# Kernel tuning notes

Hardware: AMD Instinct MI355X
Metric: run time of the kernel (lower is better)

Reference implementation:

```python
import jax, jax.numpy as jnp
import numpy as np

WIN = 7  # window side

def _relative_position_index(wh, ww):
    coords = np.stack(np.meshgrid(np.arange(wh), np.arange(ww), indexing='ij'))  # (2,wh,ww)
    coords = coords.reshape(2, -1)                       # (2, S)
    rel = coords[:, :, None] - coords[:, None, :]        # (2, S, S)
    rel = rel.transpose(1, 2, 0).copy()                  # (S, S, 2)
    rel[:, :, 0] += wh - 1
    rel[:, :, 1] += ww - 1
    rel[:, :, 0] *= 2 * ww - 1
    return rel.sum(-1).astype(np.int32)                  # (S, S)

def setup_inputs() -> dict:
    key = jax.random.key(0)
    ks = jax.random.split(key, 8)
    B_, S, D, H = 4096, WIN * WIN, 384, 6
    Wn = 64  # windows per image
    x = jax.random.normal(ks[0], (B_, S, D), dtype=jnp.float32)
    mask = jax.random.normal(ks[1], (Wn, S, S), dtype=jnp.float32)
    qkv_w = jax.random.normal(ks[2], (D, 3 * D), dtype=jnp.float32) * (D ** -0.5)
    qkv_b = jnp.zeros((3 * D,), dtype=jnp.float32)
    proj_w = jax.random.normal(ks[3], (D, D), dtype=jnp.float32) * (D ** -0.5)
    proj_b = jnp.zeros((D,), dtype=jnp.float32)
    bias_table = jax.random.normal(ks[4], ((2 * WIN - 1) ** 2, H), dtype=jnp.float32) * 0.02
    rel_index = jnp.asarray(_relative_position_index(WIN, WIN))  # (S, S) int32
    return {"x": x, "mask": mask, "qkv_w": qkv_w, "qkv_b": qkv_b,
            "proj_w": proj_w, "proj_b": proj_b, "bias_table": bias_table,
            "rel_index": rel_index}

def reference(x, mask, qkv_w, qkv_b, proj_w, proj_b, bias_table, rel_index):
    B_, S, D = x.shape
    H = bias_table.shape[1]
    hd = D // H
    scale = hd ** -0.5
    qkv = x @ qkv_w + qkv_b                              # (B_, S, 3D)
    qkv = qkv.reshape(B_, S, 3, H, hd).transpose(2, 0, 3, 1, 4)  # (3, B_, H, S, hd)
    q, k, v = qkv[0], qkv[1], qkv[2]
    attn = jnp.einsum('bhqe,bhke->bhqk', q * scale, k)   # (B_, H, S, S)
    bias = bias_table[rel_index].transpose(2, 0, 1)      # (H, S, S)
    attn = attn + bias[None]
    Wn = mask.shape[0]
    attn = attn.reshape(B_ // Wn, Wn, H, S, S) + mask[None, :, None]
    attn = jax.nn.softmax(attn.reshape(B_, H, S, S), axis=-1)
    out = jnp.einsum('bhqk,bhke->bhqe', attn, v)         # (B_, H, S, hd)
    out = out.transpose(0, 2, 1, 3).reshape(B_, S, D)
    return out @ proj_w + proj_b
```

## Files before the change

kernel.cpp:

```cpp
#include <hip/hip_runtime.h>


typedef __attribute__((ext_vector_type(8))) short bfx8;
typedef __attribute__((ext_vector_type(4))) float fx4;

typedef const __attribute__((address_space(1))) void* gptr_t;
typedef __attribute__((address_space(3))) void* lptr_t;

__device__ __forceinline__ short f2bf(float f) {
  union { float f; unsigned u; } v;
  v.f = f;
  unsigned r = v.u + 0x7fffu + ((v.u >> 16) & 1u);
  return (short)(r >> 16);
}


__global__ __launch_bounds__(256) void convT_kernel(const float* __restrict__ w,
                                                    short* __restrict__ wt, int N, int K) {
  int i = blockIdx.x * 256 + threadIdx.x;
  if (i < N * K) {
    int n = i / K, k = i - n * K;
    wt[i] = f2bf(w[(size_t)k * N + n]);
  }
}

__global__ __launch_bounds__(256) void bm_kernel(const float* __restrict__ mask,
                                                 const float* __restrict__ bias_table,
                                                 const int* __restrict__ rel_index,
                                                 float* __restrict__ bm) {
  int i = blockIdx.x * 256 + threadIdx.x;
  if (i < 64 * 6 * 2401) {
    int rc = i % 2401;
    int wh = i / 2401;
    int h = wh % 6, w = wh / 6;
    bm[i] = bias_table[rel_index[rc] * 6 + h] + mask[w * 2401 + rc];
  }
}


__global__ __launch_bounds__(256, 3) void fused_attn_kernel(
    const float* __restrict__ x,
    const short* __restrict__ wqkv_t,
    const float* __restrict__ qkv_b,
    const float* __restrict__ bm,
    short* __restrict__ O) {
  __shared__ __align__(16) short Qs[64 * 72];
  __shared__ __align__(16) short Ks[64 * 72];
  __shared__ __align__(16) short Vt[64 * 72];
  __shared__ __align__(16) short Pb[6144];
  __shared__ __align__(16) short Ws[6144];

  const int tid = threadIdx.x;
  const int lane = tid & 63, wid = tid >> 6;
  const int l15 = lane & 15, q4 = lane >> 4;
  const int b = blockIdx.x, w = b & 63;
  const float* xw = x + (size_t)b * 49 * 384;
  const float* bmp_base = bm + ((size_t)(w * 6)) * 2401;

  const fx4 zero = {0.f, 0.f, 0.f, 0.f};
  const int arow = wid * 16 + l15;
  const int crow = wid * 16 + q4 * 4;

  auto stage = [&](short* dst, int h64s, int kts) {
#pragma unroll
    for (int r = 0; r < 3; ++r) {
      const int off = r * 4096 + tid * 16;
      const int srow = off >> 6;
      const int ce = (off & 63) >> 1;
      const int n = (srow >> 6) * 384 + h64s + (srow & 63);
      __builtin_amdgcn_global_load_lds(
          (gptr_t)(wqkv_t + (size_t)n * 384 + kts * 32 + ce),
          (lptr_t)((char*)dst + off), 16, 0, 0);
    }
  };

  bfx8 af_all[12];
#pragma unroll
  for (int kt = 0; kt < 12; ++kt) {
    float4 a0 = {0.f, 0.f, 0.f, 0.f}, a1 = {0.f, 0.f, 0.f, 0.f};
    if (arow < 49) {
      const float4* ap = (const float4*)(xw + (size_t)arow * 384 + kt * 32 + q4 * 8);
      a0 = ap[0];
      a1 = ap[1];
    }
    bfx8 af;
    af[0] = f2bf(a0.x); af[1] = f2bf(a0.y); af[2] = f2bf(a0.z); af[3] = f2bf(a0.w);
    af[4] = f2bf(a1.x); af[5] = f2bf(a1.y); af[6] = f2bf(a1.z); af[7] = f2bf(a1.w);
    af_all[kt] = af;
  }

  stage(Ws, 0, 0);

  for (int h = 0; h < 6; ++h) {
    const int h64 = h * 64;
    __syncthreads();

    fx4 qacc[12];
#pragma unroll
    for (int i = 0; i < 12; ++i) qacc[i] = zero;

#pragma unroll
    for (int kt = 0; kt < 12; ++kt) {
      short* sb = (kt & 1) ? Ws : Pb;
      const short* rb = (kt & 1) ? Pb : Ws;
      if (kt < 11) stage(sb, h64, kt + 1);
      const bfx8 af = af_all[kt];
#pragma unroll
      for (int nt = 0; nt < 12; ++nt) {
        const bfx8 bf = *(const bfx8*)&rb[(nt * 16 + l15) * 32 + q4 * 8];
        qacc[nt] = __builtin_amdgcn_mfma_f32_16x16x32_bf16(af, bf, qacc[nt], 0, 0, 0);
      }
      __syncthreads();
    }

#pragma unroll
    for (int nt = 0; nt < 12; ++nt) {
      const int which = nt >> 2;
      const int e = (nt & 3) * 16 + l15;
      const float bias = qkv_b[which * 384 + h64 + e];
      const float sc = (which == 0) ? 0.125f : 1.0f;
#pragma unroll
      for (int rr = 0; rr < 4; ++rr) {
        const int row = crow + rr;
        const short v = f2bf((qacc[nt][rr] + bias) * sc);
        if (which == 0)      Qs[row * 72 + e] = v;
        else if (which == 1) Ks[row * 72 + e] = v;
        else                 Vt[e * 72 + row] = v;
      }
    }
    __syncthreads();

    if (h < 5) stage(Ws, h64 + 64, 0);

    const float* bmp = bmp_base + (size_t)h * 2401;
    float bmv[4][4];
#pragma unroll
    for (int nt = 0; nt < 4; ++nt) {
      const int c = nt * 16 + l15;
#pragma unroll
      for (int rr = 0; rr < 4; ++rr) {
        const int r = crow + rr;
        bmv[nt][rr] = (r < 49 && c < 49) ? bmp[r * 49 + c] : -1e30f;
      }
    }

    fx4 sacc[4];
#pragma unroll
    for (int i = 0; i < 4; ++i) sacc[i] = zero;
#pragma unroll
    for (int ks = 0; ks < 2; ++ks) {
      const bfx8 aq = *(const bfx8*)&Qs[arow * 72 + ks * 32 + q4 * 8];
#pragma unroll
      for (int nt = 0; nt < 4; ++nt) {
        const bfx8 bk = *(const bfx8*)&Ks[(nt * 16 + l15) * 72 + ks * 32 + q4 * 8];
        sacc[nt] = __builtin_amdgcn_mfma_f32_16x16x32_bf16(aq, bk, sacc[nt], 0, 0, 0);
      }
    }

    float p[4][4], mx[4], sm[4];
#pragma unroll
    for (int rr = 0; rr < 4; ++rr) mx[rr] = -1e30f;
#pragma unroll
    for (int nt = 0; nt < 4; ++nt)
#pragma unroll
      for (int rr = 0; rr < 4; ++rr) {
        p[nt][rr] = sacc[nt][rr] + bmv[nt][rr];
        mx[rr] = fmaxf(mx[rr], p[nt][rr]);
      }
#pragma unroll
    for (int rr = 0; rr < 4; ++rr) {
      mx[rr] = fmaxf(mx[rr], __shfl_xor(mx[rr], 1));
      mx[rr] = fmaxf(mx[rr], __shfl_xor(mx[rr], 2));
      mx[rr] = fmaxf(mx[rr], __shfl_xor(mx[rr], 4));
      mx[rr] = fmaxf(mx[rr], __shfl_xor(mx[rr], 8));
      sm[rr] = 0.f;
    }
#pragma unroll
    for (int nt = 0; nt < 4; ++nt)
#pragma unroll
      for (int rr = 0; rr < 4; ++rr) {
        const float e = __expf(p[nt][rr] - mx[rr]);
        p[nt][rr] = e;
        sm[rr] += e;
      }
#pragma unroll
    for (int rr = 0; rr < 4; ++rr) {
      sm[rr] += __shfl_xor(sm[rr], 1);
      sm[rr] += __shfl_xor(sm[rr], 2);
      sm[rr] += __shfl_xor(sm[rr], 4);
      sm[rr] += __shfl_xor(sm[rr], 8);
      sm[rr] = 1.f / sm[rr];
    }
#pragma unroll
    for (int nt = 0; nt < 4; ++nt)
#pragma unroll
      for (int rr = 0; rr < 4; ++rr)
        Pb[(crow + rr) * 72 + nt * 16 + l15] = f2bf(p[nt][rr] * sm[rr]);

    fx4 oacc[4];
#pragma unroll
    for (int i = 0; i < 4; ++i) oacc[i] = zero;
#pragma unroll
    for (int ks = 0; ks < 2; ++ks) {
      const bfx8 ap = *(const bfx8*)&Pb[arow * 72 + ks * 32 + q4 * 8];
#pragma unroll
      for (int nt = 0; nt < 4; ++nt) {
        const bfx8 bv = *(const bfx8*)&Vt[(nt * 16 + l15) * 72 + ks * 32 + q4 * 8];
        oacc[nt] = __builtin_amdgcn_mfma_f32_16x16x32_bf16(ap, bv, oacc[nt], 0, 0, 0);
      }
    }
#pragma unroll
    for (int nt = 0; nt < 4; ++nt)
#pragma unroll
      for (int rr = 0; rr < 4; ++rr) {
        const int r = crow + rr;
        if (r < 49)
          O[((size_t)b * 49 + r) * 384 + h64 + nt * 16 + l15] = f2bf(oacc[nt][rr]);
      }
  }
}


__global__ __launch_bounds__(256) void proj_kernel(
    const short* __restrict__ O,
    const short* __restrict__ wproj_t,
    const float* __restrict__ proj_b,
    float* __restrict__ out) {
  __shared__ __align__(16) short As[128 * 32];
  __shared__ __align__(16) short Bs[128 * 32];

  const int tid = threadIdx.x;
  const int lane = tid & 63, wid = tid >> 6;
  const int l15 = lane & 15, q4 = lane >> 4;
  const int tn = blockIdx.x % 3, tm = blockIdx.x / 3;
  const int wr = wid >> 1, wc = wid & 1;

  const short* Abase = O + (size_t)tm * 128 * 384;
  const short* Bbase = wproj_t + (size_t)tn * 128 * 384;

  fx4 acc[4][4];
#pragma unroll
  for (int i = 0; i < 4; ++i)
#pragma unroll
    for (int j = 0; j < 4; ++j) acc[i][j] = (fx4){0.f, 0.f, 0.f, 0.f};

  for (int kt = 0; kt < 12; ++kt) {
#pragma unroll
    for (int g = 0; g < 2; ++g) {
      const int off = g * 4096 + tid * 16;
      const int row = off >> 6;
      const int ce = (off & 63) >> 1;
      __builtin_amdgcn_global_load_lds(
          (gptr_t)(Abase + (size_t)row * 384 + kt * 32 + ce),
          (lptr_t)((char*)As + off), 16, 0, 0);
      __builtin_amdgcn_global_load_lds(
          (gptr_t)(Bbase + (size_t)row * 384 + kt * 32 + ce),
          (lptr_t)((char*)Bs + off), 16, 0, 0);
    }
    __syncthreads();
    bfx8 a[4], bf[4];
#pragma unroll
    for (int mi = 0; mi < 4; ++mi)
      a[mi] = *(const bfx8*)&As[(wr * 64 + mi * 16 + l15) * 32 + q4 * 8];
#pragma unroll
    for (int ni = 0; ni < 4; ++ni)
      bf[ni] = *(const bfx8*)&Bs[(wc * 64 + ni * 16 + l15) * 32 + q4 * 8];
#pragma unroll
    for (int mi = 0; mi < 4; ++mi)
#pragma unroll
      for (int ni = 0; ni < 4; ++ni)
        acc[mi][ni] = __builtin_amdgcn_mfma_f32_16x16x32_bf16(a[mi], bf[ni], acc[mi][ni], 0, 0, 0);
    __syncthreads();
  }

#pragma unroll
  for (int ni = 0; ni < 4; ++ni) {
    const int gn = tn * 128 + wc * 64 + ni * 16 + l15;
    const float bias = proj_b[gn];
#pragma unroll
    for (int mi = 0; mi < 4; ++mi) {
      const size_t gm = (size_t)tm * 128 + wr * 64 + mi * 16 + q4 * 4;
#pragma unroll
      for (int rr = 0; rr < 4; ++rr)
        out[(gm + rr) * 384 + gn] = acc[mi][ni][rr] + bias;
    }
  }
}


extern "C" void kernel_launch(void* const* d_in, const int* in_sizes, int n_in,
                              void* d_out, int out_size, void* d_ws, size_t ws_size,
                              hipStream_t stream) {
  const float* x       = (const float*)d_in[0];
  const float* mask    = (const float*)d_in[1];
  const float* qkv_w   = (const float*)d_in[2];
  const float* qkv_b   = (const float*)d_in[3];
  const float* proj_w  = (const float*)d_in[4];
  const float* proj_b  = (const float*)d_in[5];
  const float* bias_t  = (const float*)d_in[6];
  const int*   rel_idx = (const int*)d_in[7];
  float* out = (float*)d_out;

  char* ws = (char*)d_ws;
  short* wqkv_t  = (short*)(ws);
  short* wproj_t = (short*)(ws + 884736);
  float* bmw     = (float*)(ws + 884736 + 294912);
  short* O_ws    = (short*)(ws + 884736 + 294912 + 3687936);

  convT_kernel<<<1728, 256, 0, stream>>>(qkv_w, wqkv_t, 1152, 384);
  convT_kernel<<<576, 256, 0, stream>>>(proj_w, wproj_t, 384, 384);
  bm_kernel<<<3602, 256, 0, stream>>>(mask, bias_t, rel_idx, bmw);

  fused_attn_kernel<<<4096, 256, 0, stream>>>(x, wqkv_t, qkv_b, bmw, O_ws);
  proj_kernel<<<4704, 256, 0, stream>>>(O_ws, wproj_t, proj_b, out);
}
```

Baseline: 1.125 ms.

## Restructure fused attention QKV GEMM to keep weights in registers and x in LDS

The QKV projection is restructured: each wave now owns 16 output columns per Q/K/V and holds the full K-dimension weight fragments in registers, loading the next head's weights directly from global memory instead of staging through LDS. The input window x is converted to bf16 once into a swizzled LDS buffer that every wave reads. LDS tiles switch from padded 72-stride to XOR-swizzled 64-stride layouts to avoid bank conflicts, and barriers become explicit lgkmcnt waits plus s_barrier. The per-K-step barriers are removed, but register pressure rises sharply (36 bfx8 weight fragments), occupancy is lowered from 3 to 2 blocks, and the row-48 handling uses an extra broadcast load.

Result: slower. 2.061 ms (+83.2%).

```diff
diff --git a/kernel.cpp b/kernel.cpp
--- a/kernel.cpp
+++ b/kernel.cpp
@@ -2,6 +2,7 @@
 
 
 typedef __attribute__((ext_vector_type(8))) short bfx8;
+typedef __attribute__((ext_vector_type(4))) short bfx4;
 typedef __attribute__((ext_vector_type(4))) float fx4;
 
 typedef const __attribute__((address_space(1))) void* gptr_t;
@@ -13,6 +14,13 @@
   unsigned r = v.u + 0x7fffu + ((v.u >> 16) & 1u);
   return (short)(r >> 16);
 }
+
+#define LGKM_BARRIER()                                 \
+  do {                                                 \
+    asm volatile("s_waitcnt lgkmcnt(0)" ::: "memory"); \
+    __builtin_amdgcn_s_barrier();                      \
+    asm volatile("" ::: "memory");                     \
+  } while (0)
 
 
 __global__ __launch_bounds__(256) void convT_kernel(const float* __restrict__ w,
@@ -38,122 +46,128 @@
 }
 
 
-__global__ __launch_bounds__(256, 3) void fused_attn_kernel(
+__global__ __launch_bounds__(256, 2) void fused_attn_kernel(
     const float* __restrict__ x,
     const short* __restrict__ wqkv_t,
     const float* __restrict__ qkv_b,
     const float* __restrict__ bm,
     short* __restrict__ O) {
-  __shared__ __align__(16) short Qs[64 * 72];
-  __shared__ __align__(16) short Ks[64 * 72];
-  __shared__ __align__(16) short Vt[64 * 72];
-  __shared__ __align__(16) short Pb[6144];
-  __shared__ __align__(16) short Ws[6144];
+  __shared__ __align__(16) short xbf[49 * 384];
+  __shared__ __align__(16) short Qs[64 * 64];
+  __shared__ __align__(16) short Ks[64 * 64];
+  __shared__ __align__(16) short Vt[64 * 64];
+  __shared__ __align__(16) short Pb[64 * 64];
 
   const int tid = threadIdx.x;
   const int lane = tid & 63, wid = tid >> 6;
   const int l15 = lane & 15, q4 = lane >> 4;
   const int b = blockIdx.x, w = b & 63;
   const float* xw = x + (size_t)b * 49 * 384;
-  const float* bmp_base = bm + ((size_t)(w * 6)) * 2401;
+  const float* bmp_base = bm + (size_t)(w * 6) * 2401;
 
   const fx4 zero = {0.f, 0.f, 0.f, 0.f};
+  const bfx8 zbf = {0, 0, 0, 0, 0, 0, 0, 0};
   const int arow = wid * 16 + l15;
   const int crow = wid * 16 + q4 * 4;
-
-  auto stage = [&](short* dst, int h64s, int kts) {
-#pragma unroll
-    for (int r = 0; r < 3; ++r) {
-      const int off = r * 4096 + tid * 16;
-      const int srow = off >> 6;
-      const int ce = (off & 63) >> 1;
-      const int n = (srow >> 6) * 384 + h64s + (srow & 63);
-      __builtin_amdgcn_global_load_lds(
-          (gptr_t)(wqkv_t + (size_t)n * 384 + kts * 32 + ce),
-          (lptr_t)((char*)dst + off), 16, 0, 0);
-    }
-  };
-
-  bfx8 af_all[12];
-#pragma unroll
-  for (int kt = 0; kt < 12; ++kt) {
-    float4 a0 = {0.f, 0.f, 0.f, 0.f}, a1 = {0.f, 0.f, 0.f, 0.f};
-    if (arow < 49) {
-      const float4* ap = (const float4*)(xw + (size_t)arow * 384 + kt * 32 + q4 * 8);
-      a0 = ap[0];
-      a1 = ap[1];
-    }
-    bfx8 af;
-    af[0] = f2bf(a0.x); af[1] = f2bf(a0.y); af[2] = f2bf(a0.z); af[3] = f2bf(a0.w);
-    af[4] = f2bf(a1.x); af[5] = f2bf(a1.y); af[6] = f2bf(a1.z); af[7] = f2bf(a1.w);
-    af_all[kt] = af;
-  }
-
-  stage(Ws, 0, 0);
-
+  const int kswz = (l15 & 7) << 3;
+  const int cpart = wid * 16 + l15;
+
+  bfx8 wfrag[3][12];
+  {
+    const short* wb = wqkv_t + (size_t)(wid * 16 + l15) * 384 + q4 * 8;
+#pragma unroll
+    for (int p = 0; p < 3; ++p)
+#pragma unroll
+      for (int kt = 0; kt < 12; ++kt)
+        wfrag[p][kt] = *(const bfx8*)(wb + (size_t)p * 147456 + kt * 32);
+  }
+
+  for (int i = tid; i < 49 * 48; i += 256) {
+    const int r = i / 48, c8 = (i - r * 48) * 8;
+    const float4* ap = (const float4*)(xw + (size_t)r * 384 + c8);
+    const float4 a0 = ap[0], a1 = ap[1];
+    bfx8 v;
+    v[0] = f2bf(a0.x); v[1] = f2bf(a0.y); v[2] = f2bf(a0.z); v[3] = f2bf(a0.w);
+    v[4] = f2bf(a1.x); v[5] = f2bf(a1.y); v[6] = f2bf(a1.z); v[7] = f2bf(a1.w);
+    *(bfx8*)&xbf[r * 384 + (c8 ^ ((r & 7) << 3))] = v;
+  }
+  LGKM_BARRIER();
+
+#pragma unroll 1
   for (int h = 0; h < 6; ++h) {
-    const int h64 = h * 64;
-    __syncthreads();
-
-    fx4 qacc[12];
-#pragma unroll
-    for (int i = 0; i < 12; ++i) qacc[i] = zero;
+    fx4 qacc[3][4];
+#pragma unroll
+    for (int p = 0; p < 3; ++p)
+#pragma unroll
+      for (int mi = 0; mi < 4; ++mi) qacc[p][mi] = zero;
 
 #pragma unroll
     for (int kt = 0; kt < 12; ++kt) {
-      short* sb = (kt & 1) ? Ws : Pb;
-      const short* rb = (kt & 1) ? Pb : Ws;
-      if (kt < 11) stage(sb, h64, kt + 1);
-      const bfx8 af = af_all[kt];
-#pragma unroll
-      for (int nt = 0; nt < 12; ++nt) {
-        const bfx8 bf = *(const bfx8*)&rb[(nt * 16 + l15) * 32 + q4 * 8];
-        qacc[nt] = __builtin_amdgcn_mfma_f32_16x16x32_bf16(af, bf, qacc[nt], 0, 0, 0);
-      }
-      __syncthreads();
-    }
-
-#pragma unroll
-    for (int nt = 0; nt < 12; ++nt) {
-      const int which = nt >> 2;
-      const int e = (nt & 3) * 16 + l15;
-      const float bias = qkv_b[which * 384 + h64 + e];
-      const float sc = (which == 0) ? 0.125f : 1.0f;
-#pragma unroll
-      for (int rr = 0; rr < 4; ++rr) {
-        const int row = crow + rr;
-        const short v = f2bf((qacc[nt][rr] + bias) * sc);
-        if (which == 0)      Qs[row * 72 + e] = v;
-        else if (which == 1) Ks[row * 72 + e] = v;
-        else                 Vt[e * 72 + row] = v;
-      }
-    }
-    __syncthreads();
-
-    if (h < 5) stage(Ws, h64 + 64, 0);
+      bfx8 af[4];
+#pragma unroll
+      for (int mi = 0; mi < 3; ++mi)
+        af[mi] = *(const bfx8*)&xbf[(mi * 16 + l15) * 384 + ((kt * 32 + q4 * 8) ^ kswz)];
+      {
+        const bfx8 v48 = *(const bfx8*)&xbf[48 * 384 + kt * 32 + q4 * 8];
+        af[3] = (l15 == 0) ? v48 : zbf;
+      }
+#pragma unroll
+      for (int p = 0; p < 3; ++p)
+#pragma unroll
+        for (int mi = 0; mi < 4; ++mi)
+          qacc[p][mi] =
+              __builtin_amdgcn_mfma_f32_16x16x32_bf16(af[mi], wfrag[p][kt], qacc[p][mi], 0, 0, 0);
+    }
 
     const float* bmp = bmp_base + (size_t)h * 2401;
     float bmv[4][4];
 #pragma unroll
-    for (int nt = 0; nt < 4; ++nt) {
-      const int c = nt * 16 + l15;
-#pragma unroll
-      for (int rr = 0; rr < 4; ++rr) {
-        const int r = crow + rr;
+    for (int nt = 0; nt < 4; ++nt)
+#pragma unroll
+      for (int rr = 0; rr < 4; ++rr) {
+        const int r = crow + rr, c = nt * 16 + l15;
         bmv[nt][rr] = (r < 49 && c < 49) ? bmp[r * 49 + c] : -1e30f;
       }
-    }
+
+    if (h < 5) {
+      const short* wb = wqkv_t + (size_t)((h + 1) * 64 + wid * 16 + l15) * 384 + q4 * 8;
+#pragma unroll
+      for (int p = 0; p < 3; ++p)
+#pragma unroll
+        for (int kt = 0; kt < 12; ++kt)
+          wfrag[p][kt] = *(const bfx8*)(wb + (size_t)p * 147456 + kt * 32);
+    }
+
+    const float bq = qkv_b[h * 64 + cpart];
+    const float bk = qkv_b[384 + h * 64 + cpart];
+    const float bv = qkv_b[768 + h * 64 + cpart];
+#pragma unroll
+    for (int mi = 0; mi < 4; ++mi) {
+#pragma unroll
+      for (int rr = 0; rr < 4; ++rr) {
+        const int r = mi * 16 + q4 * 4 + rr;
+        const int cs = cpart ^ ((r & 7) << 3);
+        Qs[r * 64 + cs] = f2bf((qacc[0][mi][rr] + bq) * 0.125f);
+        Ks[r * 64 + cs] = f2bf(qacc[1][mi][rr] + bk);
+      }
+      bfx4 vv;
+#pragma unroll
+      for (int rr = 0; rr < 4; ++rr) vv[rr] = f2bf(qacc[2][mi][rr] + bv);
+      const int s0 = mi * 16 + q4 * 4;
+      *(bfx4*)&Vt[cpart * 64 + (s0 ^ kswz)] = vv;
+    }
+    LGKM_BARRIER();
 
     fx4 sacc[4];
 #pragma unroll
     for (int i = 0; i < 4; ++i) sacc[i] = zero;
 #pragma unroll
     for (int ks = 0; ks < 2; ++ks) {
-      const bfx8 aq = *(const bfx8*)&Qs[arow * 72 + ks * 32 + q4 * 8];
+      const bfx8 aq = *(const bfx8*)&Qs[arow * 64 + ((ks * 32 + q4 * 8) ^ kswz)];
 #pragma unroll
       for (int nt = 0; nt < 4; ++nt) {
-        const bfx8 bk = *(const bfx8*)&Ks[(nt * 16 + l15) * 72 + ks * 32 + q4 * 8];
-        sacc[nt] = __builtin_amdgcn_mfma_f32_16x16x32_bf16(aq, bk, sacc[nt], 0, 0, 0);
+        const bfx8 bkf = *(const bfx8*)&Ks[(nt * 16 + l15) * 64 + ((ks * 32 + q4 * 8) ^ kswz)];
+        sacc[nt] = __builtin_amdgcn_mfma_f32_16x16x32_bf16(aq, bkf, sacc[nt], 0, 0, 0);
       }
     }
 
@@ -194,19 +208,21 @@
 #pragma unroll
     for (int nt = 0; nt < 4; ++nt)
 #pragma unroll
-      for (int rr = 0; rr < 4; ++rr)
-        Pb[(crow + rr) * 72 + nt * 16 + l15] = f2bf(p[nt][rr] * sm[rr]);
+      for (int rr = 0; rr < 4; ++rr) {
+        const int r = crow + rr;
+        Pb[r * 64 + ((nt * 16 + l15) ^ ((r & 7) << 3))] = f2bf(p[nt][rr] * sm[rr]);
+      }
 
     fx4 oacc[4];
 #pragma unroll
     for (int i = 0; i < 4; ++i) oacc[i] = zero;
 #pragma unroll
     for (int ks = 0; ks < 2; ++ks) {
-      const bfx8 ap = *(const bfx8*)&Pb[arow * 72 + ks * 32 + q4 * 8];
+      const bfx8 ap = *(const bfx8*)&Pb[arow * 64 + ((ks * 32 + q4 * 8) ^ kswz)];
 #pragma unroll
       for (int nt = 0; nt < 4; ++nt) {
-        const bfx8 bv = *(const bfx8*)&Vt[(nt * 16 + l15) * 72 + ks * 32 + q4 * 8];
-        oacc[nt] = __builtin_amdgcn_mfma_f32_16x16x32_bf16(ap, bv, oacc[nt], 0, 0, 0);
+        const bfx8 bvf = *(const bfx8*)&Vt[(nt * 16 + l15) * 64 + ((ks * 32 + q4 * 8) ^ kswz)];
+        oacc[nt] = __builtin_amdgcn_mfma_f32_16x16x32_bf16(ap, bvf, oacc[nt], 0, 0, 0);
       }
     }
 #pragma unroll
@@ -215,8 +231,9 @@
       for (int rr = 0; rr < 4; ++rr) {
         const int r = crow + rr;
         if (r < 49)
-          O[((size_t)b * 49 + r) * 384 + h64 + nt * 16 + l15] = f2bf(oacc[nt][rr]);
-      }
+          O[((size_t)b * 49 + r) * 384 + h * 64 + nt * 16 + l15] = f2bf(oacc[nt][rr]);
+      }
+    LGKM_BARRIER();
   }
 }
 
```
